# Kernel tuning notes

Hardware: AMD Instinct MI355X
Metric: run time of the kernel (lower is better)

Reference implementation:

```python
import jax, jax.numpy as jnp
import numpy as np

NUM_HEADS = 16


def setup_inputs() -> dict:
    key = jax.random.key(0)
    ks = jax.random.split(key, 6)
    B, S, D = 2, 2048, 1024
    x = jax.random.normal(ks[0], (B, S, D), dtype=jnp.float32)
    # Linear weights stored as [d_in, d_out] so forward is x @ W (qkv_bias=False)
    scale = 1.0 / np.sqrt(D)
    Wq = jax.random.normal(ks[1], (D, D), dtype=jnp.float32) * scale
    Wk = jax.random.normal(ks[2], (D, D), dtype=jnp.float32) * scale
    Wv = jax.random.normal(ks[3], (D, D), dtype=jnp.float32) * scale
    Wo = jax.random.normal(ks[4], (D, D), dtype=jnp.float32) * scale
    bo = jax.random.normal(ks[5], (D,), dtype=jnp.float32) * 0.01
    return {"x": x, "Wq": Wq, "Wk": Wk, "Wv": Wv, "Wo": Wo, "bo": bo}


def reference(x, Wq, Wk, Wv, Wo, bo):
    B, S, D = x.shape
    H = NUM_HEADS
    hd = D // H

    def split_heads(t):  # [B,S,D] -> [B,H,S,hd]
        return t.reshape(B, S, H, hd).transpose(0, 2, 1, 3)

    q = split_heads(x @ Wq)
    k = split_heads(x @ Wk)
    v = split_heads(x @ Wv)

    # full score matrix [B,H,S,S]
    scores = jnp.einsum('bhsd,bhtd->bhst', q, k)
    causal = jnp.triu(jnp.ones((S, S), dtype=bool), k=1)
    scores = jnp.where(causal, -jnp.inf, scores)
    attn = jax.nn.softmax(scores * (hd ** -0.5), axis=-1)
    # dropout p=0.0 -> identity
    out = jnp.einsum('bhst,bhtd->bhsd', attn, v)
    out = out.transpose(0, 2, 1, 3).reshape(B, S, D)
    return out @ Wo + bo
```

## Files before the change

kernel.cpp:

```cpp
#include <hip/hip_runtime.h>

typedef unsigned short ushort_t;
typedef unsigned int uint_t;
typedef __attribute__((ext_vector_type(8))) short short8;
typedef __attribute__((ext_vector_type(4))) float floatx4;

#define S_LEN 2048
#define D_DIM 1024
#define H_NUM 16
#define HD 64

__device__ __forceinline__ float bf2f(ushort_t u) {
    union { uint_t i; float f; } c; c.i = ((uint_t)u) << 16; return c.f;
}
__device__ __forceinline__ ushort_t f2bf(float f) {
    union { float f; uint_t i; } c; c.f = f;
    uint_t r = c.i + 0x7fffu + ((c.i >> 16) & 1u);
    return (ushort_t)(r >> 16);
}

__device__ __forceinline__ void g2l16(const ushort_t* g, ushort_t* l) {
    __builtin_amdgcn_global_load_lds(
        (const __attribute__((address_space(1))) void*)g,
        (__attribute__((address_space(3))) void*)l, 16, 0, 0);
}

__global__ __launch_bounds__(256, 4) void cast_x_kernel(
        const float* __restrict__ in, ushort_t* __restrict__ out) {
    const int idx = (blockIdx.x * 256 + threadIdx.x) * 4;
    const float4 v = *(const float4*)(in + idx);
    ushort4 o;
    o.x = f2bf(v.x); o.y = f2bf(v.y); o.z = f2bf(v.z); o.w = f2bf(v.w);
    *(ushort4*)(out + idx) = o;
}

__global__ __launch_bounds__(256, 2) void transpose4_kernel(
        const float* __restrict__ W0, const float* __restrict__ W1,
        const float* __restrict__ W2, const float* __restrict__ W3,
        ushort_t* __restrict__ T0, ushort_t* __restrict__ T1,
        ushort_t* __restrict__ T2, ushort_t* __restrict__ T3) {
    const int z = blockIdx.z;
    const float* in  = (z == 0) ? W0 : (z == 1) ? W1 : (z == 2) ? W2 : W3;
    ushort_t*    out = (z == 0) ? T0 : (z == 1) ? T1 : (z == 2) ? T2 : T3;
    __shared__ __align__(16) ushort_t t[64][65];
    const int r0 = blockIdx.y * 64, c0 = blockIdx.x * 64;
    const int tr = threadIdx.x >> 4;
    const int tc = (threadIdx.x & 15) * 4;
#pragma unroll
    for (int i = 0; i < 4; ++i) {
        const int row = tr + i * 16;
        const float4 v = *(const float4*)(in + (size_t)(r0 + row) * D_DIM + c0 + tc);
        t[row][tc + 0] = f2bf(v.x); t[row][tc + 1] = f2bf(v.y);
        t[row][tc + 2] = f2bf(v.z); t[row][tc + 3] = f2bf(v.w);
    }
    __syncthreads();
#pragma unroll
    for (int i = 0; i < 4; ++i) {
        const int n = tr + i * 16;
        ushort4 v;
        v.x = t[tc + 0][n]; v.y = t[tc + 1][n];
        v.z = t[tc + 2][n]; v.w = t[tc + 3][n];
        *(ushort4*)(out + (size_t)(c0 + n) * D_DIM + r0 + tc) = v;
    }
}

__device__ __forceinline__ void gemm_tile(
        const ushort_t* __restrict__ A, const ushort_t* __restrict__ BT,
        const int m0, const int n0,
        ushort_t* As, ushort_t* Bs, floatx4 acc[4][4]) {
    const int tid  = threadIdx.x;
    const int w    = tid >> 6;
    const int wm   = (w >> 1) * 64;
    const int wn   = (w & 1) * 64;
    const int lrow = tid & 15;
    const int kq   = ((tid & 63) >> 4) * 8;

    const int flat0 = tid * 8;
    const int flat1 = (256 + tid) * 8;
    const int row0 = flat0 >> 5, kk0 = flat0 & 31;
    const int row1 = flat1 >> 5, kk1 = flat1 & 31;

    const ushort_t* ga0 = A  + (size_t)(m0 + row0) * D_DIM + kk0;
    const ushort_t* gb0 = BT + (size_t)(n0 + row0) * D_DIM + kk0;
    const ushort_t* ga1 = A  + (size_t)(m0 + row1) * D_DIM + kk1;
    const ushort_t* gb1 = BT + (size_t)(n0 + row1) * D_DIM + kk1;

    for (int k0 = 0; k0 < D_DIM; k0 += 32) {
        __syncthreads();
        g2l16(ga0 + k0, As + flat0);
        g2l16(gb0 + k0, Bs + flat0);
        g2l16(ga1 + k0, As + flat1);
        g2l16(gb1 + k0, Bs + flat1);
        asm volatile("s_waitcnt vmcnt(0)" ::: "memory");
        __syncthreads();

        short8 av[4], bv[4];
#pragma unroll
        for (int i = 0; i < 4; ++i)
            av[i] = *(const short8*)(As + (wm + i * 16 + lrow) * 32 + kq);
#pragma unroll
        for (int j = 0; j < 4; ++j)
            bv[j] = *(const short8*)(Bs + (wn + j * 16 + lrow) * 32 + kq);
#pragma unroll
        for (int i = 0; i < 4; ++i)
#pragma unroll
            for (int j = 0; j < 4; ++j)
                acc[i][j] = __builtin_amdgcn_mfma_f32_16x16x32_bf16(
                    av[i], bv[j], acc[i][j], 0, 0, 0);
    }
}

__global__ __launch_bounds__(256, 2) void gemm_qkv_kernel(
        const ushort_t* __restrict__ A,
        const ushort_t* __restrict__ WqT, const ushort_t* __restrict__ WkT,
        const ushort_t* __restrict__ WvT,
        ushort_t* __restrict__ Qo, ushort_t* __restrict__ Ko,
        ushort_t* __restrict__ Vo) {
    const ushort_t* BT = (blockIdx.z == 0) ? WqT : (blockIdx.z == 1) ? WkT : WvT;
    ushort_t* C        = (blockIdx.z == 0) ? Qo  : (blockIdx.z == 1) ? Ko  : Vo;
    const float sc     = (blockIdx.z == 0) ? 0.125f : 1.0f;
    __shared__ __align__(16) ushort_t As[128 * 32];
    __shared__ __align__(16) ushort_t Bs[128 * 32];
    const int m0 = blockIdx.y * 128, n0 = blockIdx.x * 128;

    floatx4 acc[4][4] = {};
    gemm_tile(A, BT, m0, n0, As, Bs, acc);

    const int tid = threadIdx.x;
    const int w = tid >> 6, wm = (w >> 1) * 64, wn = (w & 1) * 64;
    const int lrow = tid & 15;
    const int rquad = ((tid & 63) >> 4) * 4;
#pragma unroll
    for (int i = 0; i < 4; ++i) {
        const int mbase = m0 + wm + i * 16 + rquad;
#pragma unroll
        for (int j = 0; j < 4; ++j) {
            const int gn = n0 + wn + j * 16 + lrow;
#pragma unroll
            for (int r = 0; r < 4; ++r)
                C[(size_t)(mbase + r) * D_DIM + gn] = f2bf(acc[i][j][r] * sc);
        }
    }
}

__global__ __launch_bounds__(256, 2) void gemm_out_kernel(
        const ushort_t* __restrict__ A, const ushort_t* __restrict__ WoT,
        const float* __restrict__ bias, float* __restrict__ C) {
    __shared__ __align__(16) ushort_t As[128 * 32];
    __shared__ __align__(16) ushort_t Bs[128 * 32];
    const int m0 = blockIdx.y * 128, n0 = blockIdx.x * 128;

    floatx4 acc[4][4] = {};
    gemm_tile(A, WoT, m0, n0, As, Bs, acc);

    const int tid = threadIdx.x;
    const int w = tid >> 6, wm = (w >> 1) * 64, wn = (w & 1) * 64;
    const int lrow = tid & 15;
    const int rquad = ((tid & 63) >> 4) * 4;
#pragma unroll
    for (int i = 0; i < 4; ++i) {
        const int mbase = m0 + wm + i * 16 + rquad;
#pragma unroll
        for (int j = 0; j < 4; ++j) {
            const int gn = n0 + wn + j * 16 + lrow;
            const float badd = bias[gn];
#pragma unroll
            for (int r = 0; r < 4; ++r)
                C[(size_t)(mbase + r) * D_DIM + gn] = acc[i][j][r] + badd;
        }
    }
}

__global__ __launch_bounds__(256, 4) void attn_mfma_kernel(
        const ushort_t* __restrict__ Q, const ushort_t* __restrict__ K,
        const ushort_t* __restrict__ V, ushort_t* __restrict__ O) {
    __shared__ __align__(16) ushort_t Ks[64 * 64];
    __shared__ __align__(16) ushort_t Vt[64 * 64];
    __shared__ __align__(16) ushort_t Ps[4][16 * 64];

    const int bh  = blockIdx.x;
    const int b   = bh >> 4, h = bh & 15;
    const int g   = blockIdx.y & 7;
    const int p   = blockIdx.y >> 3;
    const int qt  = (p == 0) ? g : (p == 1) ? (15 - g)
                  : (p == 2) ? (16 + g) : (31 - g);
    const int q0  = qt * 64;
    const int tid = threadIdx.x;
    const int wq  = tid >> 6;
    const int lane = tid & 63;
    const int col  = lane & 15;
    const int quad = lane >> 4;
    const int c7 = col & 7;
    const int qw0  = q0 + wq * 16;
    const size_t rowbase = (size_t)b * S_LEN;
    const int ch0 = h * HD;

    const int skey = tid >> 2;
    const int schk = tid & 3;
    const int vkp = tid & 31;
    const int vdc = tid >> 5;

    short8 aq[2];
#pragma unroll
    for (int kc = 0; kc < 2; ++kc)
        aq[kc] = *(const short8*)(Q + (rowbase + qw0 + col) * D_DIM
                                    + ch0 + kc * 32 + quad * 8);

    floatx4 oacc[4] = {};
    float mrun[4], lrun[4];
#pragma unroll
    for (int r = 0; r < 4; ++r) { mrun[r] = -1e30f; lrun[r] = 0.0f; }

    const int ntiles = qt + 1;
    for (int t = 0; t < ntiles; ++t) {
        const int kb = t * 64;
        __syncthreads();
        {
            const ushort_t* kg = K + (rowbase + kb + skey) * D_DIM + ch0 + schk * 16;
            const short8 k0 = *(const short8*)(kg);
            const short8 k1 = *(const short8*)(kg + 8);
            const int sw = skey & 7;
            *(short8*)(Ks + skey * 64 + (((2 * schk) ^ sw) << 3)) = k0;
            *(short8*)(Ks + skey * 64 + (((2 * schk + 1) ^ sw) << 3)) = k1;
        }
        {
            const ushort_t* vg = V + (rowbase + kb + 2 * vkp) * D_DIM + ch0 + vdc * 8;
            const short8 v0 = *(const short8*)(vg);
            const short8 v1 = *(const short8*)(vg + D_DIM);
#pragma unroll
            for (int e = 0; e < 8; ++e) {
                const int d = vdc * 8 + e;
                const uint_t pk = (uint_t)(ushort_t)v0[e] | ((uint_t)(ushort_t)v1[e] << 16);
                *(uint_t*)(Vt + d * 64 + ((2 * vkp) ^ ((d & 7) << 3))) = pk;
            }
        }
        __syncthreads();

        if (kb <= qw0 + 15) {
            floatx4 sa[4] = {};
            __builtin_amdgcn_s_setprio(1);
#pragma unroll
            for (int kc = 0; kc < 2; ++kc)
#pragma unroll
                for (int j = 0; j < 4; ++j) {
                    const short8 bk = *(const short8*)(
                        Ks + (j * 16 + col) * 64 + (((kc * 4 + quad) ^ c7) << 3));
                    sa[j] = __builtin_amdgcn_mfma_f32_16x16x32_bf16(
                        aq[kc], bk, sa[j], 0, 0, 0);
                }
            __builtin_amdgcn_s_setprio(0);

            const bool needmask = (kb + 63 > qw0);
            if (needmask) {
#pragma unroll
                for (int j = 0; j < 4; ++j)
#pragma unroll
                    for (int r = 0; r < 4; ++r) {
                        const int row = qw0 + quad * 4 + r;
                        const int key = kb + j * 16 + col;
                        if (key > row) sa[j][r] = -1e30f;
                    }
            }
#pragma unroll
            for (int r = 0; r < 4; ++r) {
                float mx = fmaxf(fmaxf(sa[0][r], sa[1][r]),
                                 fmaxf(sa[2][r], sa[3][r]));
                mx = fmaxf(mx, __shfl_xor(mx, 1));
                mx = fmaxf(mx, __shfl_xor(mx, 2));
                mx = fmaxf(mx, __shfl_xor(mx, 4));
                mx = fmaxf(mx, __shfl_xor(mx, 8));
                const float mn = fmaxf(mrun[r], mx);
                const float al = __expf(mrun[r] - mn);
                mrun[r] = mn;
                float rs = 0.0f;
#pragma unroll
                for (int j = 0; j < 4; ++j) {
                    const float p2 = __expf(sa[j][r] - mn);
                    sa[j][r] = p2;
                    rs += p2;
                }
                lrun[r] = lrun[r] * al + rs;
#pragma unroll
                for (int jd = 0; jd < 4; ++jd) oacc[jd][r] *= al;
            }
            {
                ushort_t* pw = Ps[wq];
#pragma unroll
                for (int j = 0; j < 4; ++j)
#pragma unroll
                    for (int r = 0; r < 4; ++r) {
                        const int row = quad * 4 + r;
                        pw[row * 64 + ((j * 16 + col) ^ ((row & 7) << 3))] =
                            f2bf(sa[j][r]);
                    }
            }
            asm volatile("s_waitcnt lgkmcnt(0)" ::: "memory");
            __builtin_amdgcn_s_setprio(1);
#pragma unroll
            for (int kc = 0; kc < 2; ++kc) {
                const short8 ap = *(const short8*)(
                    Ps[wq] + col * 64 + (((kc * 4 + quad) ^ c7) << 3));
#pragma unroll
                for (int jd = 0; jd < 4; ++jd) {
                    const short8 bv = *(const short8*)(
                        Vt + (jd * 16 + col) * 64 + (((kc * 4 + quad) ^ c7) << 3));
                    oacc[jd] = __builtin_amdgcn_mfma_f32_16x16x32_bf16(
                        ap, bv, oacc[jd], 0, 0, 0);
                }
            }
            __builtin_amdgcn_s_setprio(0);
        }
    }

#pragma unroll
    for (int r = 0; r < 4; ++r) {
        float l = lrun[r];
        l += __shfl_xor(l, 1);
        l += __shfl_xor(l, 2);
        l += __shfl_xor(l, 4);
        l += __shfl_xor(l, 8);
        const int row = qw0 + quad * 4 + r;
        const float inv = 1.0f / l;
#pragma unroll
        for (int jd = 0; jd < 4; ++jd)
            O[(rowbase + row) * D_DIM + ch0 + jd * 16 + col] =
                f2bf(oacc[jd][r] * inv);
    }
}

extern "C" void kernel_launch(void* const* d_in, const int* in_sizes, int n_in,
                              void* d_out, int out_size, void* d_ws, size_t ws_size,
                              hipStream_t stream) {
    const float* x  = (const float*)d_in[0];
    const float* Wq = (const float*)d_in[1];
    const float* Wk = (const float*)d_in[2];
    const float* Wv = (const float*)d_in[3];
    const float* Wo = (const float*)d_in[4];
    const float* bo = (const float*)d_in[5];
    float* out = (float*)d_out;

    char* ws = (char*)d_ws;
    const size_t MB = 1024 * 1024;
    ushort_t* xb  = (ushort_t*)(ws + 0 * MB);
    ushort_t* WqT = (ushort_t*)(ws + 8 * MB);
    ushort_t* WkT = (ushort_t*)(ws + 10 * MB);
    ushort_t* WvT = (ushort_t*)(ws + 12 * MB);
    ushort_t* WoT = (ushort_t*)(ws + 14 * MB);
    ushort_t* Qb  = (ushort_t*)(ws + 16 * MB);
    ushort_t* Kb  = (ushort_t*)(ws + 24 * MB);
    ushort_t* Vb  = (ushort_t*)(ws + 32 * MB);
    ushort_t* Ob  = (ushort_t*)(ws + 40 * MB);

    cast_x_kernel<<<4096, 256, 0, stream>>>(x, xb);
    transpose4_kernel<<<dim3(16, 16, 4), 256, 0, stream>>>(
        Wq, Wk, Wv, Wo, WqT, WkT, WvT, WoT);

    gemm_qkv_kernel<<<dim3(8, 32, 3), 256, 0, stream>>>(
        xb, WqT, WkT, WvT, Qb, Kb, Vb);

    attn_mfma_kernel<<<dim3(32, 32), 256, 0, stream>>>(Qb, Kb, Vb, Ob);

    gemm_out_kernel<<<dim3(8, 32), 256, 0, stream>>>(Ob, WoT, bo, out);
}
```

Measured before the change: 208.5 us.

## Double-buffer GEMM LDS tiles and register-prefetch next K/V tile in attention

The shared GEMM tile loop now uses two LDS buffers and issues the global-to-LDS loads for the next K-slice before running the current slice's MFMAs, so memory latency overlaps compute. The attention kernel preloads the next K/V tile into registers while the current tile is processed, hiding global load latency behind the MFMA and softmax work. This doubles GEMM LDS usage, which may lower occupancy, and adds register pressure in attention, with one redundant extra load on the last tile.

Result: faster. 200.0 us (-4.1%).

```diff
diff --git a/kernel.cpp b/kernel.cpp
--- a/kernel.cpp
+++ b/kernel.cpp
@@ -9,6 +9,7 @@
 #define D_DIM 1024
 #define H_NUM 16
 #define HD 64
+#define GBUF (128 * 32)
 
 __device__ __forceinline__ float bf2f(ushort_t u) {
     union { uint_t i; float f; } c; c.i = ((uint_t)u) << 16; return c.f;
@@ -85,28 +86,44 @@
     const ushort_t* ga1 = A  + (size_t)(m0 + row1) * D_DIM + kk1;
     const ushort_t* gb1 = BT + (size_t)(n0 + row1) * D_DIM + kk1;
 
+    g2l16(ga0, As + flat0);
+    g2l16(gb0, Bs + flat0);
+    g2l16(ga1, As + flat1);
+    g2l16(gb1, Bs + flat1);
+    asm volatile("s_waitcnt vmcnt(0)" ::: "memory");
+    __syncthreads();
+
+    int cur = 0;
     for (int k0 = 0; k0 < D_DIM; k0 += 32) {
-        __syncthreads();
-        g2l16(ga0 + k0, As + flat0);
-        g2l16(gb0 + k0, Bs + flat0);
-        g2l16(ga1 + k0, As + flat1);
-        g2l16(gb1 + k0, Bs + flat1);
-        asm volatile("s_waitcnt vmcnt(0)" ::: "memory");
-        __syncthreads();
-
+        const ushort_t* Ac = As + cur * GBUF;
+        const ushort_t* Bc = Bs + cur * GBUF;
         short8 av[4], bv[4];
 #pragma unroll
         for (int i = 0; i < 4; ++i)
-            av[i] = *(const short8*)(As + (wm + i * 16 + lrow) * 32 + kq);
+            av[i] = *(const short8*)(Ac + (wm + i * 16 + lrow) * 32 + kq);
 #pragma unroll
         for (int j = 0; j < 4; ++j)
-            bv[j] = *(const short8*)(Bs + (wn + j * 16 + lrow) * 32 + kq);
+            bv[j] = *(const short8*)(Bc + (wn + j * 16 + lrow) * 32 + kq);
+
+        if (k0 + 32 < D_DIM) {
+            ushort_t* An = As + (cur ^ 1) * GBUF;
+            ushort_t* Bn = Bs + (cur ^ 1) * GBUF;
+            g2l16(ga0 + k0 + 32, An + flat0);
+            g2l16(gb0 + k0 + 32, Bn + flat0);
+            g2l16(ga1 + k0 + 32, An + flat1);
+            g2l16(gb1 + k0 + 32, Bn + flat1);
+        }
+
 #pragma unroll
         for (int i = 0; i < 4; ++i)
 #pragma unroll
             for (int j = 0; j < 4; ++j)
                 acc[i][j] = __builtin_amdgcn_mfma_f32_16x16x32_bf16(
                     av[i], bv[j], acc[i][j], 0, 0, 0);
+
+        asm volatile("s_waitcnt vmcnt(0)" ::: "memory");
+        __syncthreads();
+        cur ^= 1;
     }
 }
 
@@ -119,8 +136,8 @@
     const ushort_t* BT = (blockIdx.z == 0) ? WqT : (blockIdx.z == 1) ? WkT : WvT;
     ushort_t* C        = (blockIdx.z == 0) ? Qo  : (blockIdx.z == 1) ? Ko  : Vo;
     const float sc     = (blockIdx.z == 0) ? 0.125f : 1.0f;
-    __shared__ __align__(16) ushort_t As[128 * 32];
-    __shared__ __align__(16) ushort_t Bs[128 * 32];
+    __shared__ __align__(16) ushort_t As[2 * GBUF];
+    __shared__ __align__(16) ushort_t Bs[2 * GBUF];
     const int m0 = blockIdx.y * 128, n0 = blockIdx.x * 128;
 
     floatx4 acc[4][4] = {};
@@ -146,8 +163,8 @@
 __global__ __launch_bounds__(256, 2) void gemm_out_kernel(
         const ushort_t* __restrict__ A, const ushort_t* __restrict__ WoT,
         const float* __restrict__ bias, float* __restrict__ C) {
-    __shared__ __align__(16) ushort_t As[128 * 32];
-    __shared__ __align__(16) ushort_t Bs[128 * 32];
+    __shared__ __align__(16) ushort_t As[2 * GBUF];
+    __shared__ __align__(16) ushort_t Bs[2 * GBUF];
     const int m0 = blockIdx.y * 128, n0 = blockIdx.x * 128;
 
     floatx4 acc[4][4] = {};
@@ -212,27 +229,39 @@
     for (int r = 0; r < 4; ++r) { mrun[r] = -1e30f; lrun[r] = 0.0f; }
 
     const int ntiles = qt + 1;
+
+    short8 krA, krB, vrA, vrB;
+    {
+        const ushort_t* kg = K + (rowbase + skey) * D_DIM + ch0 + schk * 16;
+        krA = *(const short8*)(kg);
+        krB = *(const short8*)(kg + 8);
+        const ushort_t* vg = V + (rowbase + 2 * vkp) * D_DIM + ch0 + vdc * 8;
+        vrA = *(const short8*)(vg);
+        vrB = *(const short8*)(vg + D_DIM);
+    }
+
     for (int t = 0; t < ntiles; ++t) {
         const int kb = t * 64;
         __syncthreads();
         {
-            const ushort_t* kg = K + (rowbase + kb + skey) * D_DIM + ch0 + schk * 16;
-            const short8 k0 = *(const short8*)(kg);
-            const short8 k1 = *(const short8*)(kg + 8);
             const int sw = skey & 7;
-            *(short8*)(Ks + skey * 64 + (((2 * schk) ^ sw) << 3)) = k0;
-            *(short8*)(Ks + skey * 64 + (((2 * schk + 1) ^ sw) << 3)) = k1;
+            *(short8*)(Ks + skey * 64 + (((2 * schk) ^ sw) << 3)) = krA;
+            *(short8*)(Ks + skey * 64 + (((2 * schk + 1) ^ sw) << 3)) = krB;
+        }
+#pragma unroll
+        for (int e = 0; e < 8; ++e) {
+            const int d = vdc * 8 + e;
+            const uint_t pk = (uint_t)(ushort_t)vrA[e] | ((uint_t)(ushort_t)vrB[e] << 16);
+            *(uint_t*)(Vt + d * 64 + ((2 * vkp) ^ ((d & 7) << 3))) = pk;
         }
         {
-            const ushort_t* vg = V + (rowbase + kb + 2 * vkp) * D_DIM + ch0 + vdc * 8;
-            const short8 v0 = *(const short8*)(vg);
-            const short8 v1 = *(const short8*)(vg + D_DIM);
-#pragma unroll
-            for (int e = 0; e < 8; ++e) {
-                const int d = vdc * 8 + e;
-                const uint_t pk = (uint_t)(ushort_t)v0[e] | ((uint_t)(ushort_t)v1[e] << 16);
-                *(uint_t*)(Vt + d * 64 + ((2 * vkp) ^ ((d & 7) << 3))) = pk;
-            }
+            const int kbn = (t + 1 < ntiles) ? (t + 1) * 64 : 0;
+            const ushort_t* kg = K + (rowbase + kbn + skey) * D_DIM + ch0 + schk * 16;
+            krA = *(const short8*)(kg);
+            krB = *(const short8*)(kg + 8);
+            const ushort_t* vg = V + (rowbase + kbn + 2 * vkp) * D_DIM + ch0 + vdc * 8;
+            vrA = *(const short8*)(vg);
+            vrB = *(const short8*)(vg + D_DIM);
         }
         __syncthreads();
 
```
